# Kernel tuning notes

Hardware: AMD Instinct MI355X
Metric: run time of the kernel (lower is better)

The kernel has to match this reference:

```python
import jax, jax.numpy as jnp
import numpy as np
import math

B, LQ, LK = 4, 1024, 2048
QD, KD, VD = 768, 512, 512
H, NH = 1024, 16
HD = H // NH

def setup_inputs() -> dict:
    key = jax.random.key(0)
    ks = jax.random.split(key, 11)
    s = 0.02
    return {
        "query": jax.random.normal(ks[0], (B, LQ, QD), jnp.float32),
        "key": jax.random.normal(ks[1], (B, LK, KD), jnp.float32),
        "value": jax.random.normal(ks[2], (B, LK, VD), jnp.float32),
        "Wq": jax.random.normal(ks[3], (QD, H), jnp.float32) * s,
        "bq": jnp.zeros((H,), jnp.float32),
        "Wk": jax.random.normal(ks[4], (KD, H), jnp.float32) * s,
        "bk": jnp.zeros((H,), jnp.float32),
        "Wv": jax.random.normal(ks[5], (VD, H), jnp.float32) * s,
        "bv": jnp.zeros((H,), jnp.float32),
        "Wo": jax.random.normal(ks[6], (H, H), jnp.float32) * s,
        "bo": jnp.zeros((H,), jnp.float32),
    }

def reference(query, key, value, Wq, bq, Wk, bk, Wv, bv, Wo, bo):
    # project and split heads: [B, L, H] -> [B, NH, L, HD]
    def heads(x):
        b, l, _ = x.shape
        return x.reshape(b, l, NH, HD).transpose(0, 2, 1, 3)
    q = heads(query @ Wq + bq)   # [B, NH, LQ, HD]
    k = heads(key @ Wk + bk)     # [B, NH, LK, HD]
    v = heads(value @ Wv + bv)   # [B, NH, LK, HD]
    scores = jnp.einsum('bhqd,bhkd->bhqk', q, k) / math.sqrt(HD)
    weights = jax.nn.softmax(scores, axis=-1)  # dropout inactive (eval / rate used deterministically as identity)
    att = jnp.einsum('bhqk,bhkd->bhqd', weights, v)
    att = att.transpose(0, 2, 1, 3).reshape(query.shape[0], -1, H)
    out = att @ Wo + bo
    return out
```

## Files before the change

kernel.cpp:

```cpp
#include <hip/hip_runtime.h>
#include <math.h>

using bf16x8 = __attribute__((ext_vector_type(8))) short;
using f32x4  = __attribute__((ext_vector_type(4))) float;
using u32x2  = __attribute__((ext_vector_type(2))) unsigned int;

namespace {
constexpr int kB  = 4;
constexpr int kLQ = 1024;
constexpr int kLK = 2048;
constexpr int kH  = 1024;
constexpr int kHD = 64;
}

__device__ __forceinline__ unsigned short f2bf(float x) {
  union { float f; unsigned int u; } v; v.f = x;
  unsigned int r = v.u + 0x7fffu + ((v.u >> 16) & 1u);
  return (unsigned short)(r >> 16);
}

typedef const __attribute__((address_space(1))) unsigned int guint_t;
typedef __attribute__((address_space(3))) unsigned int luint_t;
__device__ __forceinline__ void g2l16(const void* g, void* l) {
  __builtin_amdgcn_global_load_lds(
      (guint_t*)g,
      (luint_t*)(unsigned int)(unsigned long long)l,
      16, 0, 0);
}

__global__ __launch_bounds__(256) void prep_kernel(
    const float* __restrict__ q, const float* __restrict__ k,
    const float* __restrict__ v, const float* __restrict__ Wq,
    const float* __restrict__ Wk, const float* __restrict__ Wv,
    const float* __restrict__ Wo, unsigned short* __restrict__ qo,
    unsigned short* __restrict__ ko, unsigned short* __restrict__ vo,
    unsigned short* __restrict__ WqT, unsigned short* __restrict__ WkT,
    unsigned short* __restrict__ WvT, unsigned short* __restrict__ WoT)
{
  __shared__ float tile[64][65];
  const int t = threadIdx.x;
  if (blockIdx.x < 5632) {
    int c = blockIdx.x * 256 + t;
    const float* src; unsigned short* dst;
    if (c < 393216)      { src = q; dst = qo; }
    else if (c < 917504) { src = k; dst = ko; c -= 393216; }
    else                 { src = v; dst = vo; c -= 917504; }
    const int i = c * 8;
    const float4 a = *(const float4*)(src + i);
    const float4 b = *(const float4*)(src + i + 4);
    uint4 o;
    o.x = (unsigned int)f2bf(a.x) | ((unsigned int)f2bf(a.y) << 16);
    o.y = (unsigned int)f2bf(a.z) | ((unsigned int)f2bf(a.w) << 16);
    o.z = (unsigned int)f2bf(b.x) | ((unsigned int)f2bf(b.y) << 16);
    o.w = (unsigned int)f2bf(b.z) | ((unsigned int)f2bf(b.w) << 16);
    *(uint4*)(dst + i) = o;
    return;
  }
  int id = blockIdx.x - 5632;
  const float* W; unsigned short* Wt; int Kd;
  if (id < 192)      { W = Wq; Wt = WqT; Kd = 768; }
  else if (id < 320) { W = Wk; Wt = WkT; Kd = 512;  id -= 192; }
  else if (id < 448) { W = Wv; Wt = WvT; Kd = 512;  id -= 320; }
  else               { W = Wo; Wt = WoT; Kd = 1024; id -= 448; }
  const int Nd = 1024;
  const int n0 = (id & 15) * 64;
  const int k0 = (id >> 4) * 64;
  const int rr = t >> 4;
  const int c4 = t & 15;
#pragma unroll
  for (int i = 0; i < 4; ++i) {
    const int row = i * 16 + rr;
    const float4 vv = *(const float4*)(W + (size_t)(k0 + row) * Nd + n0 + c4 * 4);
    tile[row][c4*4+0] = vv.x; tile[row][c4*4+1] = vv.y;
    tile[row][c4*4+2] = vv.z; tile[row][c4*4+3] = vv.w;
  }
  __syncthreads();
#pragma unroll
  for (int i = 0; i < 4; ++i) {
    const int n = i * 16 + rr;
    ushort4 o;
    o.x = f2bf(tile[c4*4+0][n]); o.y = f2bf(tile[c4*4+1][n]);
    o.z = f2bf(tile[c4*4+2][n]); o.w = f2bf(tile[c4*4+3][n]);
    *(ushort4*)(Wt + (size_t)(n0 + n) * Kd + k0 + c4 * 4) = o;
  }
}

__device__ __forceinline__ void gemm_body(
    const unsigned short* __restrict__ A, const unsigned short* __restrict__ Bt,
    const float* __restrict__ bias, void* __restrict__ Cout,
    int N, int K, int bx, int by, int mode, float scale, char* lds)
{
  const int t    = threadIdx.x;
  const int lane = t & 63;
  const int w    = t >> 6;
  const int l15  = lane & 15;
  const int lq8  = (lane >> 4) * 8;
  const int lq4  = (lane >> 4) * 4;
  const int r0   = by * 128;
  const int c0   = bx * 128;
  const int wm   = w >> 1, wn = w & 1;

  f32x4 acc[4][4] = {};

#pragma unroll
  for (int i = 0; i < 4; ++i) {
    const int g = w * 4 + i;
    const unsigned short* src = (g < 8) ? A : Bt;
    const int rbase = (g < 8) ? (r0 + g * 16) : (c0 + (g - 8) * 16);
    g2l16(src + (size_t)(rbase + l15) * K + lq8, lds + g * 1024 + lane * 16);
  }

  int pb = 0;
  for (int k0 = 0; k0 < K; k0 += 32, pb ^= 1) {
    __syncthreads();
    char* buf = lds + pb * 16384;
    if (k0 + 32 < K) {
      char* nbuf = lds + (pb ^ 1) * 16384;
#pragma unroll
      for (int i = 0; i < 4; ++i) {
        const int g = w * 4 + i;
        const unsigned short* src = (g < 8) ? A : Bt;
        const int rbase = (g < 8) ? (r0 + g * 16) : (c0 + (g - 8) * 16);
        g2l16(src + (size_t)(rbase + l15) * K + k0 + 32 + lq8, nbuf + g * 1024 + lane * 16);
      }
    }
    bf16x8 af[4], bfr[4];
#pragma unroll
    for (int i = 0; i < 4; ++i) af[i]  = *(const bf16x8*)(buf + (wm*4 + i) * 1024 + lane * 16);
#pragma unroll
    for (int j = 0; j < 4; ++j) bfr[j] = *(const bf16x8*)(buf + 8192 + (wn*4 + j) * 1024 + lane * 16);
#pragma unroll
    for (int i = 0; i < 4; ++i)
#pragma unroll
      for (int j = 0; j < 4; ++j)
        acc[i][j] = __builtin_amdgcn_mfma_f32_16x16x32_bf16(af[i], bfr[j], acc[i][j], 0, 0, 0);
  }

#pragma unroll
  for (int j = 0; j < 4; ++j) {
    const int col = c0 + wn * 64 + j * 16 + l15;
    const float bcol = bias[col];
#pragma unroll
    for (int i = 0; i < 4; ++i) {
      const int row = r0 + wm * 64 + i * 16 + lq4;
      if (mode == 0) {
        float* out = (float*)Cout;
#pragma unroll
        for (int r = 0; r < 4; ++r) out[(size_t)(row + r) * N + col] = acc[i][j][r] + bcol;
      } else if (mode == 1) {
        unsigned short* out = (unsigned short*)Cout;
#pragma unroll
        for (int r = 0; r < 4; ++r) out[(size_t)(row + r) * N + col] = f2bf((acc[i][j][r] + bcol) * scale);
      } else {
        unsigned short* out = (unsigned short*)Cout;
        const int bb = row >> 11;
        const int lk = row & 2047;
        ushort4 o;
        o.x = f2bf(acc[i][j][0] + bcol); o.y = f2bf(acc[i][j][1] + bcol);
        o.z = f2bf(acc[i][j][2] + bcol); o.w = f2bf(acc[i][j][3] + bcol);
        *(ushort4*)(out + (size_t)(bb * kH + col) * kLK + lk) = o;
      }
    }
  }
}

__global__ __launch_bounds__(256) void qkv_gemm_kernel(
    const unsigned short* __restrict__ qA, const unsigned short* __restrict__ WqT,
    const float* __restrict__ bq, unsigned short* __restrict__ Qb,
    const unsigned short* __restrict__ kA, const unsigned short* __restrict__ WkT,
    const float* __restrict__ bk, unsigned short* __restrict__ Kb,
    const unsigned short* __restrict__ vA, const unsigned short* __restrict__ WvT,
    const float* __restrict__ bv, unsigned short* __restrict__ Vtw)
{
  __shared__ __align__(16) char lds[32768];
  const int bid = blockIdx.x;
  int id = (bid & 7) * 160 + (bid >> 3);
  if (id < 256) {
    gemm_body(qA, WqT, bq, Qb, 1024, 768, id & 7, id >> 3, 1,
              0.18033688011112042f, lds);
  } else if (id < 768) {
    id -= 256;
    gemm_body(kA, WkT, bk, Kb, 1024, 512, id & 7, id >> 3, 1, 1.f, lds);
  } else {
    id -= 768;
    gemm_body(vA, WvT, bv, Vtw, 1024, 512, id & 7, id >> 3, 2, 1.f, lds);
  }
}

__global__ __launch_bounds__(256) void out_gemm_kernel(
    const unsigned short* __restrict__ A, const unsigned short* __restrict__ Bt,
    const float* __restrict__ bias, float* __restrict__ C)
{
  __shared__ __align__(16) char lds[32768];
  const int bid = blockIdx.x;
  const int id = (bid & 7) * 32 + (bid >> 3);
  gemm_body(A, Bt, bias, C, 1024, 1024, id & 7, id >> 3, 0, 1.f, lds);
}

__global__ __launch_bounds__(256) void attn_mfma_kernel(
    const unsigned short* __restrict__ Q, const unsigned short* __restrict__ K,
    const unsigned short* __restrict__ Vt, unsigned short* __restrict__ O)
{
  __shared__ __align__(16) char lds[51200];
  constexpr int POFF = 32768;
  const int t    = threadIdx.x;
  const int lane = t & 63;
  const int w    = t >> 6;
  const int l15  = lane & 15;
  const int lg   = lane >> 4;
  const int lq8  = lg * 8;
  const int lq4  = lg * 4;
  const int flat = blockIdx.x;
  const int bh   = flat & 63;
  const int qb   = flat >> 6;
  const int h    = bh & 15;
  const int b    = bh >> 4;
  const int q0   = qb * 128;
  const int hoff = h * kHD;

  bf16x8 qf[2][2];
#pragma unroll
  for (int qi = 0; qi < 2; ++qi)
#pragma unroll
    for (int kh = 0; kh < 2; ++kh)
      qf[qi][kh] = *(const bf16x8*)(Q + (size_t)(b*kLQ + q0 + w*32 + qi*16 + l15) * kH
                                      + hoff + kh*32 + lq8);

  f32x4 acc[2][4] = {};
  float lsum[2] = {0.f, 0.f};

  char* const pwr = lds + POFF + (w*32 + l15) * 144 + lq4 * 2;
  const char* const prd = lds + POFF + (w*32 + l15) * 144 + lq8 * 2;

#pragma unroll
  for (int i = 0; i < 4; ++i) {
    const int g = w * 4 + i;
    if (g < 8) {
      g2l16(K + (size_t)(b*kLK + (g >> 1)*16 + l15) * kH + hoff + (g & 1)*32 + lq8,
            lds + g * 1024 + lane * 16);
    } else {
      const int gg = g - 8;
      g2l16(Vt + (size_t)(b*kH + hoff + (gg >> 1)*16 + l15) * kLK + (gg & 1)*32 + lq8,
            lds + 8192 + gg * 1024 + lane * 16);
    }
  }

  int pb = 0;
  for (int kt = 0; kt < kLK / 64; ++kt, pb ^= 1) {
    __syncthreads();
    char* buf = lds + pb * 16384;
    if (kt + 1 < kLK / 64) {
      char* nbuf = lds + (pb ^ 1) * 16384;
      const int kc1 = (kt + 1) * 64;
#pragma unroll
      for (int i = 0; i < 4; ++i) {
        const int g = w * 4 + i;
        if (g < 8) {
          g2l16(K + (size_t)(b*kLK + kc1 + (g >> 1)*16 + l15) * kH + hoff + (g & 1)*32 + lq8,
                nbuf + g * 1024 + lane * 16);
        } else {
          const int gg = g - 8;
          g2l16(Vt + (size_t)(b*kH + hoff + (gg >> 1)*16 + l15) * kLK + kc1 + (gg & 1)*32 + lq8,
                nbuf + 8192 + gg * 1024 + lane * 16);
        }
      }
    }

    f32x4 s[2][4];
#pragma unroll
    for (int kcf = 0; kcf < 4; ++kcf) {
      const bf16x8 kf0 = *(const bf16x8*)(buf + (kcf*2 + 0) * 1024 + lane * 16);
      const bf16x8 kf1 = *(const bf16x8*)(buf + (kcf*2 + 1) * 1024 + lane * 16);
#pragma unroll
      for (int qi = 0; qi < 2; ++qi) {
        f32x4 z = {};
        z = __builtin_amdgcn_mfma_f32_16x16x32_bf16(kf0, qf[qi][0], z, 0, 0, 0);
        z = __builtin_amdgcn_mfma_f32_16x16x32_bf16(kf1, qf[qi][1], z, 0, 0, 0);
        s[qi][kcf] = z;
      }
    }

#pragma unroll
    for (int qi = 0; qi < 2; ++qi)
#pragma unroll
      for (int kcf = 0; kcf < 4; ++kcf) {
        const float p0 = __builtin_amdgcn_exp2f(s[qi][kcf][0]);
        const float p1 = __builtin_amdgcn_exp2f(s[qi][kcf][1]);
        const float p2 = __builtin_amdgcn_exp2f(s[qi][kcf][2]);
        const float p3 = __builtin_amdgcn_exp2f(s[qi][kcf][3]);
        lsum[qi] += (p0 + p1) + (p2 + p3);
        u32x2 pw;
        pw.x = __builtin_amdgcn_perm(__float_as_uint(p1), __float_as_uint(p0), 0x07060302u);
        pw.y = __builtin_amdgcn_perm(__float_as_uint(p3), __float_as_uint(p2), 0x07060302u);
        *(u32x2*)(pwr + qi*2304 + kcf*32) = pw;
      }

    bf16x8 pf[2][2];
#pragma unroll
    for (int qi = 0; qi < 2; ++qi)
#pragma unroll
      for (int kq = 0; kq < 2; ++kq)
        pf[qi][kq] = *(const bf16x8*)(prd + qi*2304 + kq*64);
#pragma unroll
    for (int vd = 0; vd < 4; ++vd) {
      const bf16x8 vf0 = *(const bf16x8*)(buf + 8192 + (vd*2 + 0) * 1024 + lane * 16);
      const bf16x8 vf1 = *(const bf16x8*)(buf + 8192 + (vd*2 + 1) * 1024 + lane * 16);
#pragma unroll
      for (int qi = 0; qi < 2; ++qi) {
        acc[qi][vd] = __builtin_amdgcn_mfma_f32_16x16x32_bf16(pf[qi][0], vf0, acc[qi][vd], 0, 0, 0);
        acc[qi][vd] = __builtin_amdgcn_mfma_f32_16x16x32_bf16(pf[qi][1], vf1, acc[qi][vd], 0, 0, 0);
      }
    }
  }

  float rinv[2][4];
#pragma unroll
  for (int qi = 0; qi < 2; ++qi) {
    float v = lsum[qi];
    v += __shfl_xor(v, 16);
    v += __shfl_xor(v, 32);
    v = 1.f / v;
#pragma unroll
    for (int r = 0; r < 4; ++r) rinv[qi][r] = __shfl(v, lq4 + r);
  }
#pragma unroll
  for (int qi = 0; qi < 2; ++qi)
#pragma unroll
    for (int vd = 0; vd < 4; ++vd)
#pragma unroll
      for (int r = 0; r < 4; ++r)
        O[(size_t)(b*kLQ + q0 + w*32 + qi*16 + lq4 + r) * kH + hoff + vd*16 + l15] =
            f2bf(acc[qi][vd][r] * rinv[qi][r]);
}

extern "C" void kernel_launch(void* const* d_in, const int* in_sizes, int n_in,
                              void* d_out, int out_size, void* d_ws, size_t ws_size,
                              hipStream_t stream) {
  (void)in_sizes; (void)n_in; (void)out_size; (void)ws_size;
  const float* query = (const float*)d_in[0];
  const float* key   = (const float*)d_in[1];
  const float* value = (const float*)d_in[2];
  const float* Wq = (const float*)d_in[3];
  const float* bq = (const float*)d_in[4];
  const float* Wk = (const float*)d_in[5];
  const float* bk = (const float*)d_in[6];
  const float* Wv = (const float*)d_in[7];
  const float* bv = (const float*)d_in[8];
  const float* Wo = (const float*)d_in[9];
  const float* bo = (const float*)d_in[10];
  float* out = (float*)d_out;

  unsigned short* ws  = (unsigned short*)d_ws;
  unsigned short* qA  = ws;
  unsigned short* kA  = qA  + 3145728;
  unsigned short* vA  = kA  + 4194304;
  unsigned short* WqT = vA  + 4194304;
  unsigned short* WkT = WqT + 786432;
  unsigned short* WvT = WkT + 524288;
  unsigned short* WoT = WvT + 524288;
  unsigned short* Qb  = WoT + 1048576;
  unsigned short* Kb  = Qb  + 4194304;
  unsigned short* Vtw = Kb  + 8388608;
  unsigned short* Ab  = Vtw + 8388608;

  prep_kernel<<<6336, 256, 0, stream>>>(query, key, value, Wq, Wk, Wv, Wo,
                                        qA, kA, vA, WqT, WkT, WvT, WoT);
  qkv_gemm_kernel<<<1280, 256, 0, stream>>>(qA, WqT, bq, Qb,
                                            kA, WkT, bk, Kb,
                                            vA, WvT, bv, Vtw);
  attn_mfma_kernel<<<512, 256, 0, stream>>>(Qb, Kb, Vtw, Ab);
  out_gemm_kernel<<<256, 256, 0, stream>>>(Ab, WoT, bo, out);
}
```

Measured before the change: 256.3 us.

## Triple-buffer GEMM LDS loads with vmcnt waits and drop XCD block remap

The shared GEMM body moves from double to triple buffering in LDS, issuing loads two k-steps ahead. Each step waits on the vmcnt counter (vmcnt(4)) before a raw s_barrier, instead of a full __syncthreads, so the next tile's loads can stay in flight while the current tile is computed. The block-index swizzle that grouped blocks per XCD is removed in both the QKV and output GEMM kernels, giving plain linear ordering. This raises LDS use to 48KB per block, which can lower occupancy, and the changed ordering may hurt L2 locality across XCDs.

```diff
diff --git a/kernel.cpp b/kernel.cpp
--- a/kernel.cpp
+++ b/kernel.cpp
@@ -102,27 +102,36 @@
 
   f32x4 acc[4][4] = {};
 
+  const unsigned short* gsrc[4];
+  char* ldst[4];
 #pragma unroll
   for (int i = 0; i < 4; ++i) {
     const int g = w * 4 + i;
     const unsigned short* src = (g < 8) ? A : Bt;
     const int rbase = (g < 8) ? (r0 + g * 16) : (c0 + (g - 8) * 16);
-    g2l16(src + (size_t)(rbase + l15) * K + lq8, lds + g * 1024 + lane * 16);
-  }
-
-  int pb = 0;
-  for (int k0 = 0; k0 < K; k0 += 32, pb ^= 1) {
-    __syncthreads();
-    char* buf = lds + pb * 16384;
+    gsrc[i] = src + (size_t)(rbase + l15) * K + lq8;
+    ldst[i] = lds + g * 1024 + lane * 16;
+  }
+
+#pragma unroll
+  for (int i = 0; i < 4; ++i) g2l16(gsrc[i], ldst[i]);
+#pragma unroll
+  for (int i = 0; i < 4; ++i) g2l16(gsrc[i] + 32, ldst[i] + 16384);
+
+  int slot = 0;
+  for (int k0 = 0; k0 < K; k0 += 32) {
     if (k0 + 32 < K) {
-      char* nbuf = lds + (pb ^ 1) * 16384;
-#pragma unroll
-      for (int i = 0; i < 4; ++i) {
-        const int g = w * 4 + i;
-        const unsigned short* src = (g < 8) ? A : Bt;
-        const int rbase = (g < 8) ? (r0 + g * 16) : (c0 + (g - 8) * 16);
-        g2l16(src + (size_t)(rbase + l15) * K + k0 + 32 + lq8, nbuf + g * 1024 + lane * 16);
-      }
+      asm volatile("s_waitcnt vmcnt(4)\n\ts_barrier" ::: "memory");
+    } else {
+      asm volatile("s_waitcnt vmcnt(0)\n\ts_barrier" ::: "memory");
+    }
+    char* buf = lds + slot * 16384;
+    if (k0 + 64 < K) {
+      int ns = slot + 2; if (ns >= 3) ns -= 3;
+      char* noff = ldst[0] - (lds + 0) + (char*)0; (void)noff;
+#pragma unroll
+      for (int i = 0; i < 4; ++i)
+        g2l16(gsrc[i] + k0 + 64, ldst[i] + ns * 16384);
     }
     bf16x8 af[4], bfr[4];
 #pragma unroll
@@ -134,6 +143,7 @@
 #pragma unroll
       for (int j = 0; j < 4; ++j)
         acc[i][j] = __builtin_amdgcn_mfma_f32_16x16x32_bf16(af[i], bfr[j], acc[i][j], 0, 0, 0);
+    slot = (slot == 2) ? 0 : slot + 1;
   }
 
 #pragma unroll
@@ -172,9 +182,8 @@
     const unsigned short* __restrict__ vA, const unsigned short* __restrict__ WvT,
     const float* __restrict__ bv, unsigned short* __restrict__ Vtw)
 {
-  __shared__ __align__(16) char lds[32768];
-  const int bid = blockIdx.x;
-  int id = (bid & 7) * 160 + (bid >> 3);
+  __shared__ __align__(16) char lds[49152];
+  int id = blockIdx.x;
   if (id < 256) {
     gemm_body(qA, WqT, bq, Qb, 1024, 768, id & 7, id >> 3, 1,
               0.18033688011112042f, lds);
@@ -191,9 +200,8 @@
     const unsigned short* __restrict__ A, const unsigned short* __restrict__ Bt,
     const float* __restrict__ bias, float* __restrict__ C)
 {
-  __shared__ __align__(16) char lds[32768];
-  const int bid = blockIdx.x;
-  const int id = (bid & 7) * 32 + (bid >> 3);
+  __shared__ __align__(16) char lds[49152];
+  const int id = blockIdx.x;
   gemm_body(A, Bt, bias, C, 1024, 1024, id & 7, id >> 3, 0, 1.f, lds);
 }
 
```

Measured after the change: 231.6 us. 1.11x faster.
